# Performance work log

Measured on AMD Instinct MI355X. Metric: run time of the kernel, lower is better.

## Reference

```python
import jax, jax.numpy as jnp
import numpy as np
import math

B, H, S, D = 2, 16, 2048, 64

def setup_inputs() -> dict:
    key = jax.random.key(0)
    k1, k2, k3, k4 = jax.random.split(key, 4)
    query = jax.random.normal(k1, (B, H, S, D), dtype=jnp.float32)
    key_t = jax.random.normal(k2, (B, H, S, D), dtype=jnp.float32)
    value = jax.random.normal(k3, (B, H, S, D), dtype=jnp.float32)
    mask = jax.random.randint(k4, (B, 1, 1, S), 0, 2).astype(bool)
    return {"query": query, "key": key_t, "value": value, "mask": mask}

def reference(query, key, value, mask):
    model_dim = query.shape[-1]
    q = query / jnp.asarray(math.sqrt(model_dim), query.dtype)
    # scores: [B,H,S,S]
    scores = jnp.einsum('bhqd,bhkd->bhqk', q, key)
    masking_value = -1e30 if scores.dtype == jnp.float32 else -10000.0
    scores = jnp.where(mask, jnp.asarray(masking_value, scores.dtype), scores)
    attention = jax.nn.softmax(scores, axis=-1)
    sum_value = jnp.einsum('bhqk,bhkd->bhqd', attention, value)
    return (attention, sum_value)
```

## Files before the change

kernel.cpp:

```cpp
#include <hip/hip_runtime.h>
#include <stdint.h>


#define S_DIM 2048
#define D_DIM 64
#define QT 32
#define KTILE 64
#define NKT 32
#define NT 512
#define NBH 32
#define ETS 72
#define STS 68
#define ATTN_ELEMS ((size_t)NBH * S_DIM * S_DIM)
#define QELEMS ((size_t)NBH * S_DIM * D_DIM)

typedef short s16x8 __attribute__((ext_vector_type(8)));
typedef float f32x4 __attribute__((ext_vector_type(4)));

__device__ __forceinline__ unsigned short f2bf(float x) {
  unsigned int u = __float_as_uint(x);
  u += 0x7FFF + ((u >> 16) & 1);
  return (unsigned short)(u >> 16);
}
__device__ __forceinline__ float bf2f(unsigned short h) {
  return __uint_as_float(((unsigned int)h) << 16);
}

__device__ __forceinline__ void glds16(const void* g, void* l) {
  __builtin_amdgcn_global_load_lds(
      (const __attribute__((address_space(1))) unsigned int*)g,
      (__attribute__((address_space(3))) unsigned int*)l, 16, 0, 0);
}

extern "C" __global__ __launch_bounds__(256)
void prep_kernel(const float* __restrict__ Q, const float* __restrict__ K,
                 const float* __restrict__ V, unsigned short* __restrict__ Qb,
                 unsigned short* __restrict__ Kb, unsigned short* __restrict__ Vtb) {
  __shared__ unsigned short vtl[64 * 65];
  const int t = threadIdx.x;
  const int blk = blockIdx.x;
  if (blk < 1024) {
    const int bh = blk >> 5;
    const int kt = blk & 31;
    const float* Ksrc = K + ((size_t)bh * S_DIM + kt * KTILE) * D_DIM;
    const float* Vsrc = V + ((size_t)bh * S_DIM + kt * KTILE) * D_DIM;
    unsigned short* Kdst = Kb + ((size_t)bh * S_DIM + kt * KTILE) * D_DIM;
    unsigned short* Vdst = Vtb + ((size_t)bh * S_DIM + kt * KTILE) * D_DIM;
#pragma unroll
    for (int i = 0; i < 2; ++i) {
      const int f = t + i * 256;
      const int row = f >> 3, db = f & 7;
      const float* s = Ksrc + row * 64 + db * 8;
      s16x8 v;
#pragma unroll
      for (int j = 0; j < 8; ++j) v[j] = (short)f2bf(s[j]);
      *(s16x8*)(Kdst + row * 64 + ((db * 8) ^ ((row & 7) * 8))) = v;
    }
#pragma unroll
    for (int i = 0; i < 4; ++i) {
      const int f = t + i * 256;
      const int row = f >> 4, c4 = f & 15;
      const float4 vv = *(const float4*)(Vsrc + row * 64 + c4 * 4);
      vtl[(c4 * 4 + 0) * 65 + row] = f2bf(vv.x);
      vtl[(c4 * 4 + 1) * 65 + row] = f2bf(vv.y);
      vtl[(c4 * 4 + 2) * 65 + row] = f2bf(vv.z);
      vtl[(c4 * 4 + 3) * 65 + row] = f2bf(vv.w);
    }
    __syncthreads();
#pragma unroll
    for (int i = 0; i < 2; ++i) {
      const int f = t + i * 256;
      const int d = f >> 3, b8 = f & 7;
      s16x8 v;
#pragma unroll
      for (int j = 0; j < 8; ++j) v[j] = (short)vtl[d * 65 + b8 * 8 + j];
      *(s16x8*)(Vdst + d * 64 + ((b8 * 8) ^ ((d & 7) * 8))) = v;
    }
  } else {
    const size_t base = (size_t)(blk - 1024) * 2048 + (size_t)t * 8;
    const float4 a = *(const float4*)(Q + base);
    const float4 b2 = *(const float4*)(Q + base + 4);
    s16x8 v;
    v[0] = (short)f2bf(a.x * 0.125f);  v[1] = (short)f2bf(a.y * 0.125f);
    v[2] = (short)f2bf(a.z * 0.125f);  v[3] = (short)f2bf(a.w * 0.125f);
    v[4] = (short)f2bf(b2.x * 0.125f); v[5] = (short)f2bf(b2.y * 0.125f);
    v[6] = (short)f2bf(b2.z * 0.125f); v[7] = (short)f2bf(b2.w * 0.125f);
    *(s16x8*)(Qb + base) = v;
  }
}

extern "C" __global__ __launch_bounds__(NT, 4)
void attn_kernel(const int* __restrict__ Mask, const unsigned short* __restrict__ Qb,
                 const unsigned short* __restrict__ Kb, const unsigned short* __restrict__ Vtb,
                 float* __restrict__ Out) {
  __shared__ unsigned short bufK[2][KTILE * D_DIM];
  __shared__ unsigned short bufV[2][KTILE * D_DIM];
  __shared__ unsigned short et[QT * ETS];
  __shared__ float stage[2][QT * STS];
  __shared__ float sums_part[8 * 16];
  __shared__ float inv_sums[QT];

  const int t = threadIdx.x;
  const int lane = t & 63;
  const int wave = t >> 6;
  const int l15 = lane & 15;
  const int quad = lane >> 4;
  const int tq = wave >> 2;
  const int tn = wave & 3;

  const int blk = blockIdx.x;
  const int qt_idx = blk & 63;
  const int bh = blk >> 6;
  const int q0 = qt_idx * QT;

  const char* kbase = (const char*)(Kb + (size_t)bh * S_DIM * D_DIM);
  const char* vbase = (const char*)(Vtb + (size_t)bh * S_DIM * D_DIM);
  const int* mrow = Mask + (bh >> 4) * S_DIM + tn * 16 + l15;

  const unsigned short* qrow = Qb + ((size_t)bh * S_DIM + q0 + tq * 16 + l15) * D_DIM;
  const s16x8 qf0 = *(const s16x8*)(qrow + quad * 8);
  const s16x8 qf1 = *(const s16x8*)(qrow + 32 + quad * 8);

  glds16(kbase + t * 16, (char*)bufK[0] + wave * 1024);
  glds16(vbase + t * 16, (char*)bufV[0] + wave * 1024);

  f32x4 pv = {0.f, 0.f, 0.f, 0.f};
  float rs[4] = {0.f, 0.f, 0.f, 0.f};
  unsigned int ereg[NKT][2];

  const int krow = tn * 16 + l15;
  const int sw = (l15 & 7) * 8;
  const int erow0 = tq * 16 + quad * 4;

#pragma unroll
  for (int kt = 0; kt < NKT; ++kt) {
    const int p = kt & 1;
    __syncthreads();
    const int m = mrow[kt * KTILE];
    const unsigned short* kb = bufK[p];
    f32x4 sc = {0.f, 0.f, 0.f, 0.f};
    {
      const s16x8 b0 = *(const s16x8*)(kb + krow * 64 + ((quad * 8) ^ sw));
      sc = __builtin_amdgcn_mfma_f32_16x16x32_bf16(qf0, b0, sc, 0, 0, 0);
      const s16x8 b1 = *(const s16x8*)(kb + krow * 64 + ((32 + quad * 8) ^ sw));
      sc = __builtin_amdgcn_mfma_f32_16x16x32_bf16(qf1, b1, sc, 0, 0, 0);
    }
    unsigned short e[4];
#pragma unroll
    for (int r = 0; r < 4; ++r) {
      const float ev = m ? 0.f : __expf(sc[r]);
      e[r] = f2bf(ev);
      rs[r] += bf2f(e[r]);
      et[(erow0 + r) * ETS + tn * 16 + l15] = e[r];
    }
    ereg[kt][0] = (unsigned int)e[0] | ((unsigned int)e[1] << 16);
    ereg[kt][1] = (unsigned int)e[2] | ((unsigned int)e[3] << 16);
    __syncthreads();
    if (kt + 1 < NKT) {
      glds16(kbase + (size_t)(kt + 1) * 8192 + t * 16, (char*)bufK[1 - p] + wave * 1024);
      glds16(vbase + (size_t)(kt + 1) * 8192 + t * 16, (char*)bufV[1 - p] + wave * 1024);
    }
    const unsigned short* vb = bufV[p];
    {
      const s16x8 a0 = *(const s16x8*)(et + (tq * 16 + l15) * ETS + quad * 8);
      const s16x8 b0 = *(const s16x8*)(vb + krow * 64 + ((quad * 8) ^ sw));
      pv = __builtin_amdgcn_mfma_f32_16x16x32_bf16(a0, b0, pv, 0, 0, 0);
      const s16x8 a1 = *(const s16x8*)(et + (tq * 16 + l15) * ETS + 32 + quad * 8);
      const s16x8 b1 = *(const s16x8*)(vb + krow * 64 + ((32 + quad * 8) ^ sw));
      pv = __builtin_amdgcn_mfma_f32_16x16x32_bf16(a1, b1, pv, 0, 0, 0);
    }
  }

#pragma unroll
  for (int o = 1; o < 16; o <<= 1) {
#pragma unroll
    for (int r = 0; r < 4; ++r) rs[r] += __shfl_xor(rs[r], o);
  }
  if (l15 == 0) {
#pragma unroll
    for (int r = 0; r < 4; ++r) sums_part[wave * 16 + quad * 4 + r] = rs[r];
  }
  __syncthreads();
  if (t < QT) {
    const int tqi = t >> 4, rl = t & 15;
    float s = 0.f;
#pragma unroll
    for (int w = 0; w < 4; ++w) s += sums_part[(tqi * 4 + w) * 16 + rl];
    inv_sums[t] = 1.f / fmaxf(s, 1e-30f);
  }
  __syncthreads();

  float inv_r[4];
#pragma unroll
  for (int r = 0; r < 4; ++r) inv_r[r] = inv_sums[erow0 + r];

  {
    float* svo = Out + ATTN_ELEMS + ((size_t)bh * S_DIM + q0) * D_DIM;
#pragma unroll
    for (int r = 0; r < 4; ++r)
      svo[(size_t)(erow0 + r) * D_DIM + tn * 16 + l15] = pv[r] * inv_r[r];
  }

  float* ao = Out + (size_t)bh * S_DIM * S_DIM + (size_t)q0 * S_DIM;
  const int row_t = t >> 4;
  const int c4 = t & 15;
#pragma unroll
  for (int kt = 0; kt < NKT; ++kt) {
    float* sg = stage[kt & 1];
    sg[(erow0 + 0) * STS + tn * 16 + l15] = bf2f((unsigned short)(ereg[kt][0] & 0xFFFFu)) * inv_r[0];
    sg[(erow0 + 1) * STS + tn * 16 + l15] = bf2f((unsigned short)(ereg[kt][0] >> 16)) * inv_r[1];
    sg[(erow0 + 2) * STS + tn * 16 + l15] = bf2f((unsigned short)(ereg[kt][1] & 0xFFFFu)) * inv_r[2];
    sg[(erow0 + 3) * STS + tn * 16 + l15] = bf2f((unsigned short)(ereg[kt][1] >> 16)) * inv_r[3];
    __syncthreads();
    const float4 o = *(const float4*)(sg + row_t * STS + c4 * 4);
    *(float4*)(ao + (size_t)row_t * S_DIM + kt * KTILE + c4 * 4) = o;
  }
}

extern "C" void kernel_launch(void* const* d_in, const int* in_sizes, int n_in,
                              void* d_out, int out_size, void* d_ws, size_t ws_size,
                              hipStream_t stream) {
  const float* Q = (const float*)d_in[0];
  const float* K = (const float*)d_in[1];
  const float* V = (const float*)d_in[2];
  const int* M = (const int*)d_in[3];
  float* out = (float*)d_out;
  unsigned short* Qb = (unsigned short*)d_ws;
  unsigned short* Kb = Qb + QELEMS;
  unsigned short* Vtb = Kb + QELEMS;
  hipLaunchKernelGGL(prep_kernel, dim3(3072), dim3(256), 0, stream, Q, K, V, Qb, Kb, Vtb);
  hipLaunchKernelGGL(attn_kernel, dim3(2048), dim3(NT), 0, stream, M, Qb, Kb, Vtb, out);
}
```

Measured before the change: 784.3 us.

## Write attention directly with nontemporal stores, prefetch earlier, and remap block order

The epilogue no longer stages the normalized attention tile through shared memory. Each lane now writes its probabilities straight to global memory with nontemporal scalar stores, which removes the stage buffer and one barrier per tile. The K/V prefetch for the next tile is issued at the top of each iteration so it overlaps the QK and exp work. The mid-loop barrier becomes a raw s_barrier with an explicit lgkmcnt wait, and block indices are permuted so that consecutive workgroups handle different heads. The trade-off is narrower 64-byte row segments per store instead of float4 rows. The custom barrier also does not wait on vmcnt, so correctness relies on the compiler inserting that wait at the next sync.

```diff
diff --git a/kernel.cpp b/kernel.cpp
--- a/kernel.cpp
+++ b/kernel.cpp
@@ -10,7 +10,6 @@
 #define NT 512
 #define NBH 32
 #define ETS 72
-#define STS 68
 #define ATTN_ELEMS ((size_t)NBH * S_DIM * S_DIM)
 #define QELEMS ((size_t)NBH * S_DIM * D_DIM)
 
@@ -96,7 +95,6 @@
   __shared__ unsigned short bufK[2][KTILE * D_DIM];
   __shared__ unsigned short bufV[2][KTILE * D_DIM];
   __shared__ unsigned short et[QT * ETS];
-  __shared__ float stage[2][QT * STS];
   __shared__ float sums_part[8 * 16];
   __shared__ float inv_sums[QT];
 
@@ -108,7 +106,8 @@
   const int tq = wave >> 2;
   const int tn = wave & 3;
 
-  const int blk = blockIdx.x;
+  const int blk0 = blockIdx.x;
+  const int blk = (blk0 & 7) * 256 + (blk0 >> 3);
   const int qt_idx = blk & 63;
   const int bh = blk >> 6;
   const int q0 = qt_idx * QT;
@@ -136,6 +135,10 @@
   for (int kt = 0; kt < NKT; ++kt) {
     const int p = kt & 1;
     __syncthreads();
+    if (kt + 1 < NKT) {
+      glds16(kbase + (size_t)(kt + 1) * 8192 + t * 16, (char*)bufK[1 - p] + wave * 1024);
+      glds16(vbase + (size_t)(kt + 1) * 8192 + t * 16, (char*)bufV[1 - p] + wave * 1024);
+    }
     const int m = mrow[kt * KTILE];
     const unsigned short* kb = bufK[p];
     f32x4 sc = {0.f, 0.f, 0.f, 0.f};
@@ -155,11 +158,10 @@
     }
     ereg[kt][0] = (unsigned int)e[0] | ((unsigned int)e[1] << 16);
     ereg[kt][1] = (unsigned int)e[2] | ((unsigned int)e[3] << 16);
-    __syncthreads();
-    if (kt + 1 < NKT) {
-      glds16(kbase + (size_t)(kt + 1) * 8192 + t * 16, (char*)bufK[1 - p] + wave * 1024);
-      glds16(vbase + (size_t)(kt + 1) * 8192 + t * 16, (char*)bufV[1 - p] + wave * 1024);
-    }
+    __builtin_amdgcn_sched_barrier(0);
+    asm volatile("s_waitcnt lgkmcnt(0)" ::: "memory");
+    __builtin_amdgcn_s_barrier();
+    __builtin_amdgcn_sched_barrier(0);
     const unsigned short* vb = bufV[p];
     {
       const s16x8 a0 = *(const s16x8*)(et + (tq * 16 + l15) * ETS + quad * 8);
@@ -198,22 +200,22 @@
     float* svo = Out + ATTN_ELEMS + ((size_t)bh * S_DIM + q0) * D_DIM;
 #pragma unroll
     for (int r = 0; r < 4; ++r)
-      svo[(size_t)(erow0 + r) * D_DIM + tn * 16 + l15] = pv[r] * inv_r[r];
-  }
-
-  float* ao = Out + (size_t)bh * S_DIM * S_DIM + (size_t)q0 * S_DIM;
-  const int row_t = t >> 4;
-  const int c4 = t & 15;
+      __builtin_nontemporal_store(pv[r] * inv_r[r],
+                                  svo + (size_t)(erow0 + r) * D_DIM + tn * 16 + l15);
+  }
+
+  float* ao = Out + (size_t)bh * S_DIM * S_DIM + (size_t)q0 * S_DIM + tn * 16 + l15;
 #pragma unroll
   for (int kt = 0; kt < NKT; ++kt) {
-    float* sg = stage[kt & 1];
-    sg[(erow0 + 0) * STS + tn * 16 + l15] = bf2f((unsigned short)(ereg[kt][0] & 0xFFFFu)) * inv_r[0];
-    sg[(erow0 + 1) * STS + tn * 16 + l15] = bf2f((unsigned short)(ereg[kt][0] >> 16)) * inv_r[1];
-    sg[(erow0 + 2) * STS + tn * 16 + l15] = bf2f((unsigned short)(ereg[kt][1] & 0xFFFFu)) * inv_r[2];
-    sg[(erow0 + 3) * STS + tn * 16 + l15] = bf2f((unsigned short)(ereg[kt][1] >> 16)) * inv_r[3];
-    __syncthreads();
-    const float4 o = *(const float4*)(sg + row_t * STS + c4 * 4);
-    *(float4*)(ao + (size_t)row_t * S_DIM + kt * KTILE + c4 * 4) = o;
+    float* col = ao + kt * KTILE;
+    __builtin_nontemporal_store(bf2f((unsigned short)(ereg[kt][0] & 0xFFFFu)) * inv_r[0],
+                                col + (size_t)(erow0 + 0) * S_DIM);
+    __builtin_nontemporal_store(bf2f((unsigned short)(ereg[kt][0] >> 16)) * inv_r[1],
+                                col + (size_t)(erow0 + 1) * S_DIM);
+    __builtin_nontemporal_store(bf2f((unsigned short)(ereg[kt][1] & 0xFFFFu)) * inv_r[2],
+                                col + (size_t)(erow0 + 2) * S_DIM);
+    __builtin_nontemporal_store(bf2f((unsigned short)(ereg[kt][1] >> 16)) * inv_r[3],
+                                col + (size_t)(erow0 + 3) * S_DIM);
   }
 }
 
```

Result: faster. 737.8 us (-5.9%).
